# Performance work log

Hardware: AMD Instinct MI355X
Metric: run time of the kernel (lower is better)

Reference implementation:

```python
import jax, jax.numpy as jnp
import numpy as np

N = 50000      # num_nodes
E = 800000     # num_edges (avg degree 16)
IC, OC = 2, 2  # in_channels, out_channels
DIN, DOUT = 128, 128
K = 3          # number of hops


def setup_inputs() -> dict:
    key = jax.random.key(0)
    k1, k2, k3, k4 = jax.random.split(key, 4)
    x = jax.random.normal(k1, (IC, N, DIN), dtype=jnp.float32)
    edge_index = jax.random.randint(k2, (2, E), 0, N, dtype=jnp.int32)
    a = np.sqrt(6.0 / (DIN + DOUT)).astype(np.float32)  # xavier_uniform bound
    W = jax.random.uniform(k3, (OC, IC, DIN, DOUT), minval=-a, maxval=a, dtype=jnp.float32)
    params = jax.random.uniform(k4, (OC, IC, K + 1), minval=0.0, maxval=0.01, dtype=jnp.float32)
    return {"x": x, "edge_index": edge_index, "W": W, "params": params}


def reference(x, edge_index, W, params):
    # x: [IC, N, DIN]; edge_index: [2, E]; W: [OC, IC, DIN, DOUT]; params: [OC, IC, K+1]
    n = x.shape[1]
    k_hops = params.shape[-1] - 1
    row, col = edge_index[0], edge_index[1]

    # normalize_adj: symmetric D^-1/2 A D^-1/2 on unit-valued edges
    deg = jax.ops.segment_sum(jnp.ones(row.shape[0], x.dtype), row, num_segments=n)
    dinv = jnp.where(deg > 0, jax.lax.rsqrt(deg), jnp.zeros_like(deg))
    val = dinv[row] * dinv[col]  # [E]

    def spmm(X):  # A_norm @ X per channel; X: [IC, N, d]
        gathered = X[:, col, :] * val[None, :, None]  # [IC, E, d]
        return jax.vmap(lambda g: jax.ops.segment_sum(g, row, num_segments=n))(gathered)

    # Hop features: H[m] = A^m x, computed once (hoisting the redundant spmm in the torch loop)
    hops = [x]
    for _ in range(k_hops):
        hops.append(spmm(hops[-1]))
    H = jnp.stack(hops)  # [K+1, IC, N, DIN]

    # out[i] = sum_j sum_m params[i,j,m] * (A^m x_j) @ W[i,j]
    return jnp.einsum('mjnd,ijm,ijdf->inf', H, params, W)  # [OC, N, DOUT]
```

## Files before the change

### kernel.cpp

```cpp
#include <hip/hip_runtime.h>
#include <hip/hip_bf16.h>
#include <stdint.h>

#define NN 50000
#define NE 800000
#define D 128
#define KH 3
#define SCAN_B ((NN + 255) / 256)

typedef __attribute__((ext_vector_type(8))) __bf16 bf16x8;
typedef __attribute__((ext_vector_type(4))) float f32x4;

__device__ __forceinline__ uint16_t bf16_rne(float f) {
  uint32_t u = __builtin_bit_cast(uint32_t, f);
  u = (u + 0x7fffu + ((u >> 16) & 1u)) >> 16;
  return (uint16_t)u;
}

#define GLDS16(gp, lp)                                                         \
  __builtin_amdgcn_global_load_lds(                                            \
      (__attribute__((address_space(1))) void*)(gp),                           \
      (__attribute__((address_space(3))) void*)(lp), 16, 0, 0)

__global__ void k_deg(const int* __restrict__ row, int* __restrict__ deg) {
  int e = blockIdx.x * 256 + threadIdx.x;
  if (e < NE) atomicAdd(&deg[row[e]], 1);
}

__global__ void k_dinv(const int* __restrict__ deg, float* __restrict__ dinv) {
  int i = blockIdx.x * 256 + threadIdx.x;
  if (i < NN) {
    int d = deg[i];
    dinv[i] = (d > 0) ? rsqrtf((float)d) : 0.0f;
  }
}

__global__ void k_bsum(const int* __restrict__ deg, int* __restrict__ bsum) {
  __shared__ int s[256];
  int t = threadIdx.x;
  int i = blockIdx.x * 256 + t;
  s[t] = (i < NN) ? deg[i] : 0;
  __syncthreads();
  for (int off = 128; off > 0; off >>= 1) {
    if (t < off) s[t] += s[t + off];
    __syncthreads();
  }
  if (t == 0) bsum[blockIdx.x] = s[0];
}

__global__ void k_bscan(const int* __restrict__ bsum, int* __restrict__ boff) {
  __shared__ int s[256];
  int t = threadIdx.x;
  int v = (t < SCAN_B) ? bsum[t] : 0;
  s[t] = v;
  __syncthreads();
  for (int off = 1; off < 256; off <<= 1) {
    int u = (t >= off) ? s[t - off] : 0;
    __syncthreads();
    s[t] += u;
    __syncthreads();
  }
  boff[t] = s[t] - v;
}

__global__ void k_rpwrite(const int* __restrict__ deg, const int* __restrict__ boff,
                          int* __restrict__ rp, int* __restrict__ cur) {
  __shared__ int s[256];
  int t = threadIdx.x;
  int i = blockIdx.x * 256 + t;
  int v = (i < NN) ? deg[i] : 0;
  s[t] = v;
  __syncthreads();
  for (int off = 1; off < 256; off <<= 1) {
    int u = (t >= off) ? s[t - off] : 0;
    __syncthreads();
    s[t] += u;
    __syncthreads();
  }
  if (i < NN) {
    int r = boff[blockIdx.x] + s[t] - v;
    rp[i] = r;
    cur[i] = r;
  }
  if (i == 0) rp[NN] = NE;
}

__global__ void k_scatter(const int* __restrict__ row, const int* __restrict__ col,
                          const float* __restrict__ dinv, int* __restrict__ cur,
                          int2* __restrict__ csr) {
  int e = blockIdx.x * 256 + threadIdx.x;
  if (e < NE) {
    int r = row[e], c = col[e];
    int pos = atomicAdd(&cur[r], 1);
    csr[pos] = make_int2(c, __float_as_int(dinv[r] * dinv[c]));
  }
}

__global__ void k_wbig_c(const float* __restrict__ W, const float* __restrict__ params,
                         uint16_t* __restrict__ wb) {
  int idx = blockIdx.x * 256 + threadIdx.x;
  if (idx >= 256 * 1024) return;
  int c = idx >> 10, k = idx & 1023;
  int i = c >> 7, f = c & 127, m = k >> 8, j = (k >> 7) & 1, dd = k & 127;
  float p = params[(i * 2 + j) * 4 + m];
  float w = W[((i * 2 + j) * 128 + dd) * 128 + f];
  wb[idx] = bf16_rne(p * w);
}

__global__ void k_wbig_f(const float* __restrict__ W, const float* __restrict__ params,
                         uint16_t* __restrict__ wb) {
  int idx = blockIdx.x * 256 + threadIdx.x;
  if (idx >= 2 * 256 * 512) return;
  int j = idx >> 17, c = (idx >> 9) & 255, k = idx & 511;
  int i = c >> 7, f = c & 127, m = k >> 7, dd = k & 127;
  float p = params[(i * 2 + j) * 4 + m];
  float w = W[((i * 2 + j) * 128 + dd) * 128 + f];
  wb[idx] = bf16_rne(p * w);
}

__global__ void k_x2h_c(const float* __restrict__ x, uint16_t* __restrict__ dst) {
  int idx = blockIdx.x * 256 + threadIdx.x;
  if (idx >= NN * 256) return;
  int n = idx >> 8, c = idx & 255, j = c >> 7, dd = c & 127;
  dst[idx] = bf16_rne(x[(size_t)j * NN * D + (size_t)n * D + dd]);
}

__global__ void k_x2h_f(const float* __restrict__ xj, uint16_t* __restrict__ dst) {
  int idx = blockIdx.x * 256 + threadIdx.x;
  if (idx < NN * D) dst[idx] = bf16_rne(xj[idx]);
}

template <int NCH>
__global__ void k_spmm(const int* __restrict__ rp, const int2* __restrict__ csr,
                       const uint16_t* __restrict__ src, uint16_t* __restrict__ dst) {
  constexpr int STRIDE = NCH * 128;
  typedef uint32_t gvec __attribute__((ext_vector_type(NCH)));
  const int lane = threadIdx.x & 63;
  const int wid = threadIdx.x >> 6;
  const int r = blockIdx.x * 4 + wid;
  if (r >= NN) return;
  const int s = __builtin_amdgcn_readfirstlane(rp[r]);
  const int e = __builtin_amdgcn_readfirstlane(rp[r + 1]);
  const int lo = lane * 2 * NCH;

  float a[2 * NCH] = {};
  int i = s;
  for (; i + 4 <= e; i += 4) {
    int2 c0 = csr[i], c1 = csr[i + 1], c2 = csr[i + 2], c3 = csr[i + 3];
    gvec g0 = *(const gvec*)(src + (size_t)c0.x * STRIDE + lo);
    gvec g1 = *(const gvec*)(src + (size_t)c1.x * STRIDE + lo);
    gvec g2 = *(const gvec*)(src + (size_t)c2.x * STRIDE + lo);
    gvec g3 = *(const gvec*)(src + (size_t)c3.x * STRIDE + lo);
    float v0 = __int_as_float(c0.y), v1 = __int_as_float(c1.y);
    float v2 = __int_as_float(c2.y), v3 = __int_as_float(c3.y);
#pragma unroll
    for (int q = 0; q < NCH; ++q) {
      a[2 * q] = fmaf(v0, __builtin_bit_cast(float, g0[q] << 16), a[2 * q]);
      a[2 * q + 1] = fmaf(v0, __builtin_bit_cast(float, g0[q] & 0xffff0000u), a[2 * q + 1]);
      a[2 * q] = fmaf(v1, __builtin_bit_cast(float, g1[q] << 16), a[2 * q]);
      a[2 * q + 1] = fmaf(v1, __builtin_bit_cast(float, g1[q] & 0xffff0000u), a[2 * q + 1]);
      a[2 * q] = fmaf(v2, __builtin_bit_cast(float, g2[q] << 16), a[2 * q]);
      a[2 * q + 1] = fmaf(v2, __builtin_bit_cast(float, g2[q] & 0xffff0000u), a[2 * q + 1]);
      a[2 * q] = fmaf(v3, __builtin_bit_cast(float, g3[q] << 16), a[2 * q]);
      a[2 * q + 1] = fmaf(v3, __builtin_bit_cast(float, g3[q] & 0xffff0000u), a[2 * q + 1]);
    }
  }
  for (; i < e; ++i) {
    int2 cv = csr[i];
    float val = __int_as_float(cv.y);
    gvec g = *(const gvec*)(src + (size_t)cv.x * STRIDE + lo);
#pragma unroll
    for (int q = 0; q < NCH; ++q) {
      a[2 * q] = fmaf(val, __builtin_bit_cast(float, g[q] << 16), a[2 * q]);
      a[2 * q + 1] = fmaf(val, __builtin_bit_cast(float, g[q] & 0xffff0000u), a[2 * q + 1]);
    }
  }
  gvec o;
#pragma unroll
  for (int q = 0; q < NCH; ++q)
    o[q] = ((uint32_t)bf16_rne(a[2 * q + 1]) << 16) | (uint32_t)bf16_rne(a[2 * q]);
  *(gvec*)(dst + (size_t)r * STRIDE + lo) = o;
}

template <int KTOT, int HOPW, int ACCUM>
__global__ __launch_bounds__(256) void k_gemm(
    const uint16_t* __restrict__ h0, const uint16_t* __restrict__ h1,
    const uint16_t* __restrict__ h2, const uint16_t* __restrict__ h3,
    const uint16_t* __restrict__ wb, float* __restrict__ out) {
  __shared__ __align__(16) uint16_t As[128 * 32];
  __shared__ __align__(16) uint16_t Bs[128 * 32];
  int t = threadIdx.x;
  int lane = t & 63, wid = t >> 6;
  int wm = wid >> 1, wn = wid & 1;
  int m0 = blockIdx.x * 128;
  int c0 = blockIdx.y * 128;
  int rl = lane & 15, kq = (lane >> 4) * 8;
  f32x4 acc[4][4] = {};
  for (int k0 = 0; k0 < KTOT; k0 += 32) {
    int hop = k0 / HOPW, kin = k0 % HOPW;
    const uint16_t* hm = hop == 0 ? h0 : hop == 1 ? h1 : hop == 2 ? h2 : h3;
#pragma unroll
    for (int rr = 0; rr < 2; ++rr) {
      int c = rr * 256 + t;
      int row = c >> 2, kc = c & 3;
      int gr = m0 + row;
      gr = gr < NN ? gr : NN - 1;
      GLDS16(hm + (size_t)gr * HOPW + kin + kc * 8, &As[c * 8]);
    }
#pragma unroll
    for (int rr = 0; rr < 2; ++rr) {
      int c = rr * 256 + t;
      int cc = c >> 2, kc = c & 3;
      GLDS16(wb + (size_t)(c0 + cc) * KTOT + k0 + kc * 8, &Bs[c * 8]);
    }
    __syncthreads();
    bf16x8 af[4], bq[4];
#pragma unroll
    for (int f = 0; f < 4; ++f)
      af[f] = *(const bf16x8*)(&As[(wm * 64 + f * 16 + rl) * 32 + kq]);
#pragma unroll
    for (int f = 0; f < 4; ++f)
      bq[f] = *(const bf16x8*)(&Bs[(wn * 64 + f * 16 + rl) * 32 + kq]);
#pragma unroll
    for (int fm = 0; fm < 4; ++fm)
#pragma unroll
      for (int fn = 0; fn < 4; ++fn)
        acc[fm][fn] = __builtin_amdgcn_mfma_f32_16x16x32_bf16(af[fm], bq[fn],
                                                              acc[fm][fn], 0, 0, 0);
    __syncthreads();
  }
  int iOut = blockIdx.y;
#pragma unroll
  for (int fm = 0; fm < 4; ++fm) {
#pragma unroll
    for (int r = 0; r < 4; ++r) {
      int rowg = m0 + wm * 64 + fm * 16 + (lane >> 4) * 4 + r;
      if (rowg >= NN) continue;
      float* op = out + ((size_t)iOut * NN + rowg) * D;
#pragma unroll
      for (int fn = 0; fn < 4; ++fn) {
        int colg = wn * 64 + fn * 16 + rl;
        if (ACCUM)
          op[colg] += acc[fm][fn][r];
        else
          op[colg] = acc[fm][fn][r];
      }
    }
  }
}

extern "C" void kernel_launch(void* const* d_in, const int* in_sizes, int n_in,
                              void* d_out, int out_size, void* d_ws, size_t ws_size,
                              hipStream_t stream) {
  (void)in_sizes; (void)n_in; (void)out_size;
  const float* x = (const float*)d_in[0];
  const int* ei = (const int*)d_in[1];
  const float* W = (const float*)d_in[2];
  const float* params = (const float*)d_in[3];
  float* out = (float*)d_out;
  char* ws = (char*)d_ws;

  size_t off = 0;
  auto take = [&](size_t bytes) {
    char* p = ws + off;
    off = (off + bytes + 255) & ~(size_t)255;
    return p;
  };
  int* deg = (int*)take((size_t)NN * 4);
  float* dinv = (float*)take((size_t)NN * 4);
  int* rp = (int*)take((size_t)(NN + 1) * 4);
  int* cur = (int*)take((size_t)NN * 4);
  int* bsum = (int*)take(256 * 4);
  int* boff = (int*)take(256 * 4);
  int2* csr = (int2*)take((size_t)NE * 8);
  uint16_t* wb = (uint16_t*)take((size_t)256 * 1024 * 2);
  size_t fixed = off;

  hipMemsetAsync(deg, 0, (size_t)NN * 4, stream);
  k_deg<<<(NE + 255) / 256, 256, 0, stream>>>(ei, deg);
  k_dinv<<<(NN + 255) / 256, 256, 0, stream>>>(deg, dinv);
  k_bsum<<<SCAN_B, 256, 0, stream>>>(deg, bsum);
  k_bscan<<<1, 256, 0, stream>>>(bsum, boff);
  k_rpwrite<<<SCAN_B, 256, 0, stream>>>(deg, boff, rp, cur);
  k_scatter<<<(NE + 255) / 256, 256, 0, stream>>>(ei, ei + NE, dinv, cur, csr);

  size_t hopC = (size_t)NN * 256 * 2;
  size_t needC = fixed + 4 * hopC + 1024;

  if (ws_size >= needC) {
    uint16_t* hop[4];
    for (int m = 0; m < 4; ++m) hop[m] = (uint16_t*)take(hopC);
    k_wbig_c<<<(256 * 1024 + 255) / 256, 256, 0, stream>>>(W, params, wb);
    k_x2h_c<<<(NN * 256 + 255) / 256, 256, 0, stream>>>(x, hop[0]);
    for (int m = 1; m <= KH; ++m)
      k_spmm<2><<<(NN + 3) / 4, 256, 0, stream>>>(rp, csr, hop[m - 1], hop[m]);
    dim3 grid((NN + 127) / 128, 2);
    k_gemm<1024, 256, 0><<<grid, 256, 0, stream>>>(hop[0], hop[1], hop[2], hop[3],
                                                   wb, out);
  } else {
    size_t hopF = (size_t)NN * 128 * 2;
    uint16_t* hop[4];
    for (int m = 0; m < 4; ++m) hop[m] = (uint16_t*)take(hopF);
    k_wbig_f<<<(2 * 256 * 512 + 255) / 256, 256, 0, stream>>>(W, params, wb);
    for (int j = 0; j < 2; ++j) {
      k_x2h_f<<<(NN * D + 255) / 256, 256, 0, stream>>>(x + (size_t)j * NN * D, hop[0]);
      for (int m = 1; m <= KH; ++m)
        k_spmm<1><<<(NN + 3) / 4, 256, 0, stream>>>(rp, csr, hop[m - 1], hop[m]);
      dim3 grid((NN + 127) / 128, 2);
      if (j == 0)
        k_gemm<512, 128, 0><<<grid, 256, 0, stream>>>(hop[0], hop[1], hop[2], hop[3],
                                                      wb, out);
      else
        k_gemm<512, 128, 1><<<grid, 256, 0, stream>>>(hop[0], hop[1], hop[2], hop[3],
                                                      wb + 256 * 512, out);
    }
  }
}
```

Measured before the change: 422.0 us.

## Fuse prep kernels, deepen SpMM gather unroll, swizzle GEMM LDS layout

Merges the dinv and block-sum kernels into one, and merges the x-to-bf16 conversion with the weight-premultiply kernel, which removes two launches. The SpMM inner loop now issues 8 neighbor gathers at once before doing the FMAs, so more memory requests are in flight per wave. The GEMM stores its LDS tiles with an XOR swizzle on the 16-byte chunk index to reduce bank conflicts, and unrolls the hop loop so the hop pointer is chosen at compile time. The wider SpMM unroll raises register use, which could lower occupancy.

```diff
diff --git a/kernel.cpp b/kernel.cpp
--- a/kernel.cpp
+++ b/kernel.cpp
@@ -27,19 +27,14 @@
   if (e < NE) atomicAdd(&deg[row[e]], 1);
 }
 
-__global__ void k_dinv(const int* __restrict__ deg, float* __restrict__ dinv) {
-  int i = blockIdx.x * 256 + threadIdx.x;
-  if (i < NN) {
-    int d = deg[i];
-    dinv[i] = (d > 0) ? rsqrtf((float)d) : 0.0f;
-  }
-}
-
-__global__ void k_bsum(const int* __restrict__ deg, int* __restrict__ bsum) {
+__global__ void k_dinv_bsum(const int* __restrict__ deg, float* __restrict__ dinv,
+                            int* __restrict__ bsum) {
   __shared__ int s[256];
   int t = threadIdx.x;
   int i = blockIdx.x * 256 + t;
-  s[t] = (i < NN) ? deg[i] : 0;
+  int d = (i < NN) ? deg[i] : 0;
+  if (i < NN) dinv[i] = (d > 0) ? rsqrtf((float)d) : 0.0f;
+  s[t] = d;
   __syncthreads();
   for (int off = 128; off > 0; off >>= 1) {
     if (t < off) s[t] += s[t + off];
@@ -96,15 +91,22 @@
   }
 }
 
-__global__ void k_wbig_c(const float* __restrict__ W, const float* __restrict__ params,
+__global__ void k_prep_c(const float* __restrict__ x, const float* __restrict__ W,
+                         const float* __restrict__ params, uint16_t* __restrict__ dst,
                          uint16_t* __restrict__ wb) {
-  int idx = blockIdx.x * 256 + threadIdx.x;
-  if (idx >= 256 * 1024) return;
-  int c = idx >> 10, k = idx & 1023;
-  int i = c >> 7, f = c & 127, m = k >> 8, j = (k >> 7) & 1, dd = k & 127;
-  float p = params[(i * 2 + j) * 4 + m];
-  float w = W[((i * 2 + j) * 128 + dd) * 128 + f];
-  wb[idx] = bf16_rne(p * w);
+  int b = blockIdx.x, t = threadIdx.x;
+  if (b < NN) {
+    int idx = b * 256 + t;
+    int n = idx >> 8, c = idx & 255, j = c >> 7, dd = c & 127;
+    dst[idx] = bf16_rne(x[(size_t)j * NN * D + (size_t)n * D + dd]);
+  } else {
+    int idx = (b - NN) * 256 + t;
+    int c = idx >> 10, k = idx & 1023;
+    int i = c >> 7, f = c & 127, m = k >> 8, j = (k >> 7) & 1, dd = k & 127;
+    float p = params[(i * 2 + j) * 4 + m];
+    float w = W[((i * 2 + j) * 128 + dd) * 128 + f];
+    wb[idx] = bf16_rne(p * w);
+  }
 }
 
 __global__ void k_wbig_f(const float* __restrict__ W, const float* __restrict__ params,
@@ -116,13 +118,6 @@
   float p = params[(i * 2 + j) * 4 + m];
   float w = W[((i * 2 + j) * 128 + dd) * 128 + f];
   wb[idx] = bf16_rne(p * w);
-}
-
-__global__ void k_x2h_c(const float* __restrict__ x, uint16_t* __restrict__ dst) {
-  int idx = blockIdx.x * 256 + threadIdx.x;
-  if (idx >= NN * 256) return;
-  int n = idx >> 8, c = idx & 255, j = c >> 7, dd = c & 127;
-  dst[idx] = bf16_rne(x[(size_t)j * NN * D + (size_t)n * D + dd]);
 }
 
 __global__ void k_x2h_f(const float* __restrict__ xj, uint16_t* __restrict__ dst) {
@@ -145,34 +140,52 @@
 
   float a[2 * NCH] = {};
   int i = s;
+  for (; i + 8 <= e; i += 8) {
+    int2 cv[8];
+    gvec g[8];
+#pragma unroll
+    for (int u = 0; u < 8; ++u) cv[u] = csr[i + u];
+#pragma unroll
+    for (int u = 0; u < 8; ++u)
+      g[u] = *(const gvec*)(src + (size_t)cv[u].x * STRIDE + lo);
+#pragma unroll
+    for (int u = 0; u < 8; ++u) {
+      float v = __int_as_float(cv[u].y);
+#pragma unroll
+      for (int q = 0; q < NCH; ++q) {
+        a[2 * q] = fmaf(v, __builtin_bit_cast(float, g[u][q] << 16), a[2 * q]);
+        a[2 * q + 1] =
+            fmaf(v, __builtin_bit_cast(float, g[u][q] & 0xffff0000u), a[2 * q + 1]);
+      }
+    }
+  }
   for (; i + 4 <= e; i += 4) {
-    int2 c0 = csr[i], c1 = csr[i + 1], c2 = csr[i + 2], c3 = csr[i + 3];
-    gvec g0 = *(const gvec*)(src + (size_t)c0.x * STRIDE + lo);
-    gvec g1 = *(const gvec*)(src + (size_t)c1.x * STRIDE + lo);
-    gvec g2 = *(const gvec*)(src + (size_t)c2.x * STRIDE + lo);
-    gvec g3 = *(const gvec*)(src + (size_t)c3.x * STRIDE + lo);
-    float v0 = __int_as_float(c0.y), v1 = __int_as_float(c1.y);
-    float v2 = __int_as_float(c2.y), v3 = __int_as_float(c3.y);
-#pragma unroll
-    for (int q = 0; q < NCH; ++q) {
-      a[2 * q] = fmaf(v0, __builtin_bit_cast(float, g0[q] << 16), a[2 * q]);
-      a[2 * q + 1] = fmaf(v0, __builtin_bit_cast(float, g0[q] & 0xffff0000u), a[2 * q + 1]);
-      a[2 * q] = fmaf(v1, __builtin_bit_cast(float, g1[q] << 16), a[2 * q]);
-      a[2 * q + 1] = fmaf(v1, __builtin_bit_cast(float, g1[q] & 0xffff0000u), a[2 * q + 1]);
-      a[2 * q] = fmaf(v2, __builtin_bit_cast(float, g2[q] << 16), a[2 * q]);
-      a[2 * q + 1] = fmaf(v2, __builtin_bit_cast(float, g2[q] & 0xffff0000u), a[2 * q + 1]);
-      a[2 * q] = fmaf(v3, __builtin_bit_cast(float, g3[q] << 16), a[2 * q]);
-      a[2 * q + 1] = fmaf(v3, __builtin_bit_cast(float, g3[q] & 0xffff0000u), a[2 * q + 1]);
+    int2 cv[4];
+    gvec g[4];
+#pragma unroll
+    for (int u = 0; u < 4; ++u) cv[u] = csr[i + u];
+#pragma unroll
+    for (int u = 0; u < 4; ++u)
+      g[u] = *(const gvec*)(src + (size_t)cv[u].x * STRIDE + lo);
+#pragma unroll
+    for (int u = 0; u < 4; ++u) {
+      float v = __int_as_float(cv[u].y);
+#pragma unroll
+      for (int q = 0; q < NCH; ++q) {
+        a[2 * q] = fmaf(v, __builtin_bit_cast(float, g[u][q] << 16), a[2 * q]);
+        a[2 * q + 1] =
+            fmaf(v, __builtin_bit_cast(float, g[u][q] & 0xffff0000u), a[2 * q + 1]);
+      }
     }
   }
   for (; i < e; ++i) {
     int2 cv = csr[i];
-    float val = __int_as_float(cv.y);
+    float v = __int_as_float(cv.y);
     gvec g = *(const gvec*)(src + (size_t)cv.x * STRIDE + lo);
 #pragma unroll
     for (int q = 0; q < NCH; ++q) {
-      a[2 * q] = fmaf(val, __builtin_bit_cast(float, g[q] << 16), a[2 * q]);
-      a[2 * q + 1] = fmaf(val, __builtin_bit_cast(float, g[q] & 0xffff0000u), a[2 * q + 1]);
+      a[2 * q] = fmaf(v, __builtin_bit_cast(float, g[q] << 16), a[2 * q]);
+      a[2 * q + 1] = fmaf(v, __builtin_bit_cast(float, g[q] & 0xffff0000u), a[2 * q + 1]);
     }
   }
   gvec o;
@@ -189,52 +202,64 @@
     const uint16_t* __restrict__ wb, float* __restrict__ out) {
   __shared__ __align__(16) uint16_t As[128 * 32];
   __shared__ __align__(16) uint16_t Bs[128 * 32];
+  const uint16_t* hops[4] = {h0, h1, h2, h3};
   int t = threadIdx.x;
   int lane = t & 63, wid = t >> 6;
   int wm = wid >> 1, wn = wid & 1;
   int m0 = blockIdx.x * 128;
   int c0 = blockIdx.y * 128;
-  int rl = lane & 15, kq = (lane >> 4) * 8;
+  int rl = lane & 15, q = lane >> 4;
   f32x4 acc[4][4] = {};
-  for (int k0 = 0; k0 < KTOT; k0 += 32) {
-    int hop = k0 / HOPW, kin = k0 % HOPW;
-    const uint16_t* hm = hop == 0 ? h0 : hop == 1 ? h1 : hop == 2 ? h2 : h3;
-#pragma unroll
-    for (int rr = 0; rr < 2; ++rr) {
-      int c = rr * 256 + t;
-      int row = c >> 2, kc = c & 3;
-      int gr = m0 + row;
-      gr = gr < NN ? gr : NN - 1;
-      GLDS16(hm + (size_t)gr * HOPW + kin + kc * 8, &As[c * 8]);
-    }
-#pragma unroll
-    for (int rr = 0; rr < 2; ++rr) {
-      int c = rr * 256 + t;
-      int cc = c >> 2, kc = c & 3;
-      GLDS16(wb + (size_t)(c0 + cc) * KTOT + k0 + kc * 8, &Bs[c * 8]);
-    }
-    __syncthreads();
-    bf16x8 af[4], bq[4];
-#pragma unroll
-    for (int f = 0; f < 4; ++f)
-      af[f] = *(const bf16x8*)(&As[(wm * 64 + f * 16 + rl) * 32 + kq]);
-#pragma unroll
-    for (int f = 0; f < 4; ++f)
-      bq[f] = *(const bf16x8*)(&Bs[(wn * 64 + f * 16 + rl) * 32 + kq]);
-#pragma unroll
-    for (int fm = 0; fm < 4; ++fm)
-#pragma unroll
-      for (int fn = 0; fn < 4; ++fn)
-        acc[fm][fn] = __builtin_amdgcn_mfma_f32_16x16x32_bf16(af[fm], bq[fn],
-                                                              acc[fm][fn], 0, 0, 0);
-    __syncthreads();
+#pragma unroll
+  for (int hop = 0; hop < KTOT / HOPW; ++hop) {
+    const uint16_t* hm = hops[hop];
+    for (int kin = 0; kin < HOPW; kin += 32) {
+      int k0 = hop * HOPW + kin;
+#pragma unroll
+      for (int rr = 0; rr < 2; ++rr) {
+        int c = rr * 256 + t;
+        int row = c >> 2, kcL = c & 3;
+        int kcG = kcL ^ (row & 3);
+        int gr = m0 + row;
+        gr = gr < NN ? gr : NN - 1;
+        GLDS16(hm + (size_t)gr * HOPW + kin + kcG * 8, &As[c * 8]);
+      }
+#pragma unroll
+      for (int rr = 0; rr < 2; ++rr) {
+        int c = rr * 256 + t;
+        int cc = c >> 2, kcL = c & 3;
+        int kcG = kcL ^ (cc & 3);
+        GLDS16(wb + (size_t)(c0 + cc) * KTOT + k0 + kcG * 8, &Bs[c * 8]);
+      }
+      __syncthreads();
+      bf16x8 af[4], bq[4];
+#pragma unroll
+      for (int f = 0; f < 4; ++f) {
+        int row = wm * 64 + f * 16 + rl;
+        int kc = q ^ (rl & 3);
+        af[f] = *(const bf16x8*)(&As[row * 32 + kc * 8]);
+      }
+#pragma unroll
+      for (int f = 0; f < 4; ++f) {
+        int row = wn * 64 + f * 16 + rl;
+        int kc = q ^ (rl & 3);
+        bq[f] = *(const bf16x8*)(&Bs[row * 32 + kc * 8]);
+      }
+#pragma unroll
+      for (int fm = 0; fm < 4; ++fm)
+#pragma unroll
+        for (int fn = 0; fn < 4; ++fn)
+          acc[fm][fn] = __builtin_amdgcn_mfma_f32_16x16x32_bf16(af[fm], bq[fn],
+                                                                acc[fm][fn], 0, 0, 0);
+      __syncthreads();
+    }
   }
   int iOut = blockIdx.y;
 #pragma unroll
   for (int fm = 0; fm < 4; ++fm) {
 #pragma unroll
     for (int r = 0; r < 4; ++r) {
-      int rowg = m0 + wm * 64 + fm * 16 + (lane >> 4) * 4 + r;
+      int rowg = m0 + wm * 64 + fm * 16 + q * 4 + r;
       if (rowg >= NN) continue;
       float* op = out + ((size_t)iOut * NN + rowg) * D;
 #pragma unroll
@@ -278,8 +303,7 @@
 
   hipMemsetAsync(deg, 0, (size_t)NN * 4, stream);
   k_deg<<<(NE + 255) / 256, 256, 0, stream>>>(ei, deg);
-  k_dinv<<<(NN + 255) / 256, 256, 0, stream>>>(deg, dinv);
-  k_bsum<<<SCAN_B, 256, 0, stream>>>(deg, bsum);
+  k_dinv_bsum<<<SCAN_B, 256, 0, stream>>>(deg, dinv, bsum);
   k_bscan<<<1, 256, 0, stream>>>(bsum, boff);
   k_rpwrite<<<SCAN_B, 256, 0, stream>>>(deg, boff, rp, cur);
   k_scatter<<<(NE + 255) / 256, 256, 0, stream>>>(ei, ei + NE, dinv, cur, csr);
@@ -290,8 +314,7 @@
   if (ws_size >= needC) {
     uint16_t* hop[4];
     for (int m = 0; m < 4; ++m) hop[m] = (uint16_t*)take(hopC);
-    k_wbig_c<<<(256 * 1024 + 255) / 256, 256, 0, stream>>>(W, params, wb);
-    k_x2h_c<<<(NN * 256 + 255) / 256, 256, 0, stream>>>(x, hop[0]);
+    k_prep_c<<<NN + 1024, 256, 0, stream>>>(x, W, params, hop[0], wb);
     for (int m = 1; m <= KH; ++m)
       k_spmm<2><<<(NN + 3) / 4, 256, 0, stream>>>(rp, csr, hop[m - 1], hop[m]);
     dim3 grid((NN + 127) / 128, 2);
```

After: 417.0 us. Within noise of the previous version (-1.2%).
